# Optimization experiments

Hardware: AMD Instinct MI355X
Metric: run time of the kernel (lower is better)

## Reference

```python
import jax, jax.numpy as jnp
import numpy as np

HID, HEADS = 1024, 16
HEAD_DIM = HID // HEADS

def _rope_table(seq_len, d):
    inv_freq = 1.0 / (10000.0 ** (jnp.arange(0, d, 2, dtype=jnp.float32) / d))  # [d/2]
    sin_inp = jnp.arange(seq_len, dtype=jnp.float32)[:, None] * inv_freq[None, :]  # [S, d/2]
    return jnp.concatenate([jnp.sin(sin_inp), jnp.cos(sin_inp)], axis=-1)  # [S, d]

def _apply_rope(x, pos_emb):
    # Faithful to original: cos/sin of the (already sin/cos) pos_emb values.
    half = x.shape[-1] // 2
    x1, x2 = x[..., :half], x[..., half:]
    p1, p2 = pos_emb[..., :half], pos_emb[..., half:]
    return jnp.concatenate([x1 * jnp.cos(p1) + x2 * jnp.sin(p1),
                            x2 * jnp.cos(p2) - x1 * jnp.sin(p2)], axis=-1)

def setup_inputs() -> dict:
    key = jax.random.key(0)
    ks = jax.random.split(key, 11)
    B, S = 8, 1024
    s = 1.0 / np.sqrt(HID)
    return {
        'query': jax.random.normal(ks[0], (B, S, HID), jnp.float32),
        'key':   jax.random.normal(ks[1], (B, S, HID), jnp.float32),
        'value': jax.random.normal(ks[2], (B, S, HID), jnp.float32),
        'Wq': jax.random.normal(ks[3], (HID, HID), jnp.float32) * s,
        'bq': jax.random.normal(ks[4], (HID,), jnp.float32) * s,
        'Wk': jax.random.normal(ks[5], (HID, HID), jnp.float32) * s,
        'bk': jax.random.normal(ks[6], (HID,), jnp.float32) * s,
        'Wv': jax.random.normal(ks[7], (HID, HID), jnp.float32) * s,
        'bv': jax.random.normal(ks[8], (HID,), jnp.float32) * s,
        'Wo': jax.random.normal(ks[9], (HID, HID), jnp.float32) * s,
        'bo': jax.random.normal(ks[10], (HID,), jnp.float32) * s,
    }

def reference(query, key, value, Wq, bq, Wk, bk, Wv, bv, Wo, bo):
    B, S, _ = query.shape
    q = query @ Wq.T + bq
    k = key @ Wk.T + bk
    v = value @ Wv.T + bv
    pos_emb = _rope_table(S, HID)
    q = _apply_rope(q, pos_emb)
    k = _apply_rope(k, pos_emb)
    v = _apply_rope(v, pos_emb)  # original applies RoPE to V too
    # split heads: [B, H, S, D]
    q = q.reshape(B, S, HEADS, HEAD_DIM).transpose(0, 2, 1, 3)
    k = k.reshape(B, S, HEADS, HEAD_DIM).transpose(0, 2, 1, 3)
    v = v.reshape(B, S, HEADS, HEAD_DIM).transpose(0, 2, 1, 3)
    scale = jnp.sqrt(jnp.float32(HEAD_DIM))
    attn = jnp.einsum('bhqd,bhkd->bhqk', q, k) / scale
    attn = jax.nn.softmax(attn, axis=-1)  # dropout=0.0 (eval): identity
    x = jnp.einsum('bhqk,bhkd->bhqd', attn, v)
    x = x.transpose(0, 2, 1, 3).reshape(B, S, HID)
    return x @ Wo.T + bo
```

## Files before the change

kernel.cpp:

```cpp
#include <hip/hip_runtime.h>
#include <hip/hip_fp16.h>
#include <cmath>


typedef _Float16 f16;
typedef __attribute__((ext_vector_type(4))) _Float16 f16x4;
typedef __attribute__((ext_vector_type(8))) _Float16 f16x8;
typedef __attribute__((ext_vector_type(4))) float f32x4;

#define MFMA16(a, b, c) __builtin_amdgcn_mfma_f32_16x16x32_f16((a), (b), (c), 0, 0, 0)
#define MFMA16K16(a, b, c) __builtin_amdgcn_mfma_f32_16x16x16f16((a), (b), (c), 0, 0, 0)

__device__ __forceinline__ void g2l16(void* lds, const void* g) {
  __builtin_amdgcn_global_load_lds(
      (const __attribute__((address_space(1))) void*)g,
      (__attribute__((address_space(3))) void*)lds,
      16, 0, 0);
}

__global__ void cvt3_kernel(const float* __restrict__ a, const float* __restrict__ b,
                            const float* __restrict__ c,
                            f16* __restrict__ oa, f16* __restrict__ ob, f16* __restrict__ oc) {
  const float* src;
  f16* dst;
  if (blockIdx.y == 0) { src = a; dst = oa; }
  else if (blockIdx.y == 1) { src = b; dst = ob; }
  else { src = c; dst = oc; }
  size_t t = (size_t)blockIdx.x * 256 + threadIdx.x;
  float4 v = ((const float4*)src)[t];
  f16x4 w = { (f16)v.x, (f16)v.y, (f16)v.z, (f16)v.w };
  ((f16x4*)dst)[t] = w;
}

__global__ void cvt4_kernel(const float* __restrict__ a, const float* __restrict__ b,
                            const float* __restrict__ c, const float* __restrict__ d,
                            f16* __restrict__ oa, f16* __restrict__ ob,
                            f16* __restrict__ oc, f16* __restrict__ od) {
  const float* src;
  f16* dst;
  if (blockIdx.y == 0) { src = a; dst = oa; }
  else if (blockIdx.y == 1) { src = b; dst = ob; }
  else if (blockIdx.y == 2) { src = c; dst = oc; }
  else { src = d; dst = od; }
  size_t t = (size_t)blockIdx.x * 256 + threadIdx.x;
  float4 v = ((const float4*)src)[t];
  f16x4 w = { (f16)v.x, (f16)v.y, (f16)v.z, (f16)v.w };
  ((f16x4*)dst)[t] = w;
}

struct GemmBatch {
  const f16* A[3];
  const f16* W[3];
  const float* bias[3];
  void* O[3];
  float scale[3];
};

template <bool OUT_F16>
__global__ __launch_bounds__(256)
void gemm_f16_kernel(GemmBatch gb) {
  __shared__ __align__(16) f16 sA[128 * 64];
  __shared__ __align__(16) f16 sB[128 * 64];
  const int z = blockIdx.z;
  const f16* __restrict__ A = gb.A[z];
  const f16* __restrict__ Bw = gb.W[z];
  const float* __restrict__ bias = gb.bias[z];
  void* __restrict__ Out = gb.O[z];
  const float sc = gb.scale[z];

  const int tid = threadIdx.x;
  const int lane = tid & 63;
  const int wv = tid >> 6;
  const int l15 = lane & 15;
  const int quad = lane >> 4;

  const int flat = blockIdx.x + (blockIdx.y << 3);
  const int xcd = flat & 7;
  const int t64 = flat >> 3;
  const int m0 = (xcd * 8 + (t64 & 7)) * 128;
  const int n0 = (t64 >> 3) * 128;

  const int wm = (wv & 1) * 64;
  const int wn = (wv >> 1) * 64;

  const int srow = lane >> 3;
  const int schunk = (lane & 7) ^ srow;
  const f16* gA = A + (size_t)(m0 + wv * 32 + srow) * 1024 + schunk * 8;
  const f16* gB = Bw + (size_t)(n0 + wv * 32 + srow) * 1024 + schunk * 8;
  f16* lA = sA + (wv * 32) * 64;
  f16* lB = sB + (wv * 32) * 64;

  f32x4 acc[4][4] = {};

  for (int k0 = 0; k0 < 1024; k0 += 64) {
    __syncthreads();
#pragma unroll
    for (int j = 0; j < 4; ++j) {
      g2l16(lA + j * 8 * 64, gA + (size_t)j * 8 * 1024 + k0);
      g2l16(lB + j * 8 * 64, gB + (size_t)j * 8 * 1024 + k0);
    }
    __syncthreads();
#pragma unroll
    for (int kc = 0; kc < 2; ++kc) {
      f16x8 af[4], bf[4];
#pragma unroll
      for (int t = 0; t < 4; ++t) {
        const int swz = ((kc * 4 + quad) ^ (l15 & 7)) * 8;
        af[t] = *(const f16x8*)(sA + (wm + t * 16 + l15) * 64 + swz);
        bf[t] = *(const f16x8*)(sB + (wn + t * 16 + l15) * 64 + swz);
      }
#pragma unroll
      for (int mi = 0; mi < 4; ++mi)
#pragma unroll
        for (int ni = 0; ni < 4; ++ni)
          acc[mi][ni] = MFMA16(af[mi], bf[ni], acc[mi][ni]);
    }
  }

#pragma unroll
  for (int ni = 0; ni < 4; ++ni) {
    const int col = n0 + wn + ni * 16 + l15;
    const float bv = bias[col];
#pragma unroll
    for (int mi = 0; mi < 4; ++mi) {
      const int row0 = m0 + wm + mi * 16 + quad * 4;
#pragma unroll
      for (int r = 0; r < 4; ++r) {
        float v = (acc[mi][ni][r] + bv) * sc;
        if (OUT_F16)
          ((f16*)Out)[(size_t)(row0 + r) * 1024 + col] = (f16)v;
        else
          ((float*)Out)[(size_t)(row0 + r) * 1024 + col] = v;
      }
    }
  }
}

__global__ __launch_bounds__(256)
void rope_kernel(f16* __restrict__ q, f16* __restrict__ k,
                 const f16* __restrict__ v, f16* __restrict__ vt) {
  __shared__ f16 sT[128 * 72];
  const int t = threadIdx.x;
  const int c0 = blockIdx.x * 64;
  const int s0 = blockIdx.y * 64;
  const int b = blockIdx.z;
  const int sr = t >> 2;
  const int cq = (t & 3) * 16;
  const int s = s0 + sr;

  float c1[16], s1[16], c2[16], s2[16];
#pragma unroll
  for (int j = 0; j < 16; ++j) {
    const int i = c0 + cq + j;
    const float invf = exp2f((float)i * -0.025952563241307517f);
    const float th = (float)s * invf;
    const float p1 = sinf(th), p2 = cosf(th);
    c1[j] = __cosf(p1); s1[j] = __sinf(p1);
    c2[j] = __cosf(p2); s2[j] = __sinf(p2);
  }

  const size_t base = ((size_t)(b * 1024 + s)) * 1024 + c0 + cq;

#pragma unroll
  for (int tz = 0; tz < 2; ++tz) {
    f16* ptr = tz ? k : q;
    f16x8 x1a = *(f16x8*)(ptr + base);
    f16x8 x1b = *(f16x8*)(ptr + base + 8);
    f16x8 x2a = *(f16x8*)(ptr + base + 512);
    f16x8 x2b = *(f16x8*)(ptr + base + 520);
    f16x8 r1a, r1b, r2a, r2b;
#pragma unroll
    for (int j = 0; j < 8; ++j) {
      float a0 = (float)x1a[j], b0 = (float)x2a[j];
      float a1 = (float)x1b[j], b1 = (float)x2b[j];
      r1a[j] = (f16)(a0 * c1[j] + b0 * s1[j]);
      r2a[j] = (f16)(b0 * c2[j] - a0 * s2[j]);
      r1b[j] = (f16)(a1 * c1[8 + j] + b1 * s1[8 + j]);
      r2b[j] = (f16)(b1 * c2[8 + j] - a1 * s2[8 + j]);
    }
    *(f16x8*)(ptr + base) = r1a;
    *(f16x8*)(ptr + base + 8) = r1b;
    *(f16x8*)(ptr + base + 512) = r2a;
    *(f16x8*)(ptr + base + 520) = r2b;
  }

  {
    f16x8 x1a = *(const f16x8*)(v + base);
    f16x8 x1b = *(const f16x8*)(v + base + 8);
    f16x8 x2a = *(const f16x8*)(v + base + 512);
    f16x8 x2b = *(const f16x8*)(v + base + 520);
#pragma unroll
    for (int j = 0; j < 8; ++j) {
      float a0 = (float)x1a[j], b0 = (float)x2a[j];
      float a1 = (float)x1b[j], b1 = (float)x2b[j];
      sT[(cq + j) * 72 + sr] = (f16)(a0 * c1[j] + b0 * s1[j]);
      sT[(64 + cq + j) * 72 + sr] = (f16)(b0 * c2[j] - a0 * s2[j]);
      sT[(cq + 8 + j) * 72 + sr] = (f16)(a1 * c1[8 + j] + b1 * s1[8 + j]);
      sT[(64 + cq + 8 + j) * 72 + sr] = (f16)(b1 * c2[8 + j] - a1 * s2[8 + j]);
    }
  }
  __syncthreads();

  const int lr = t >> 1;
  const int sh = (t & 1) * 32;
  const int h = (lr < 64) ? (c0 >> 6) : (8 + (c0 >> 6));
  const int d = lr & 63;
  const size_t gbase = ((size_t)((b * 16 + h) * 64 + d)) * 1024 + s0 + sh;
#pragma unroll
  for (int m = 0; m < 4; ++m)
    *(f16x8*)(vt + gbase + m * 8) = *(const f16x8*)(sT + lr * 72 + sh + m * 8);
}

__global__ __launch_bounds__(512, 8)
void attn_kernel(const f16* __restrict__ q, const f16* __restrict__ k,
                 const f16* __restrict__ vt, f16* __restrict__ xo) {
  __shared__ __align__(16) f16 smem[16384];
  f16* sK = smem;
  f16* sV = smem + 128 * 64;
  const int tid = threadIdx.x;
  const int lane = tid & 63;
  const int wv = tid >> 6;
  const int l15 = lane & 15;
  const int quad = lane >> 4;
  const int bh = blockIdx.x;
  const int qt = blockIdx.y;
  const int b = bh >> 4, h = bh & 15;
  const size_t hidbase = ((size_t)b << 20) + (size_t)(h << 6);
  const int sq0 = qt * 128 + wv * 16;

  f16x8 fq[2];
#pragma unroll
  for (int kc = 0; kc < 2; ++kc)
    fq[kc] = *(const f16x8*)(q + hidbase + (size_t)(sq0 + l15) * 1024 + kc * 32 + quad * 8);

  f32x4 ot[4] = {};
  f32x4 ls = {};
  const f16x4 fone = { (f16)1.0f, (f16)1.0f, (f16)1.0f, (f16)1.0f };

  const int srowK = lane >> 3;
  const int schunkK = (lane & 7) ^ srowK;
  const f16* gK = k + hidbase + (size_t)(wv * 16 + srowK) * 1024 + schunkK * 8;
  const int vrow = lane >> 4;
  const f16* gVbase = vt + ((size_t)bh * 64) * 1024;

  for (int kt = 0; kt < 8; ++kt) {
    const int sk0 = kt * 128;
    __syncthreads();
#pragma unroll
    for (int j = 0; j < 2; ++j)
      g2l16(sK + (wv * 16 + j * 8) * 64, gK + (size_t)(sk0 + j * 8) * 1024);
#pragma unroll
    for (int i = 0; i < 2; ++i) {
      const int row = wv * 8 + i * 4 + vrow;
      const int gch = (lane & 15) ^ (row & 15);
      g2l16(sV + (wv * 8 + i * 4) * 128, gVbase + (size_t)row * 1024 + sk0 + gch * 8);
    }
    __syncthreads();

#pragma unroll
    for (int nj = 0; nj < 8; ++nj) {
      f32x4 st = { -12.0f, -12.0f, -12.0f, -12.0f };
#pragma unroll
      for (int kc = 0; kc < 2; ++kc) {
        f16x8 fk = *(const f16x8*)(sK + (nj * 16 + l15) * 64 +
                                   ((kc * 4 + quad) ^ (l15 & 7)) * 8);
        st = MFMA16(fk, fq[kc], st);
      }
      const float p0 = exp2f(st[0]);
      const float p1 = exp2f(st[1]);
      const float p2 = exp2f(st[2]);
      const float p3 = exp2f(st[3]);
      auto plo = __builtin_amdgcn_cvt_pkrtz(p0, p1);
      auto phi = __builtin_amdgcn_cvt_pkrtz(p2, p3);
      f16x4 pf;
      pf[0] = (f16)plo[0]; pf[1] = (f16)plo[1];
      pf[2] = (f16)phi[0]; pf[3] = (f16)phi[1];
      ls = MFMA16K16(fone, pf, ls);
#pragma unroll
      for (int nd = 0; nd < 4; ++nd) {
        f16x4 fv = *(const f16x4*)(sV + (nd * 16 + l15) * 128 +
                                   ((nj * 2 + (quad >> 1)) ^ l15) * 8 + (quad & 1) * 4);
        ot[nd] = MFMA16K16(fv, pf, ot[nd]);
      }
    }
  }

  const float inv = 1.0f / ls[0];

  __syncthreads();
  f16* sO = smem + wv * (16 * 72);
#pragma unroll
  for (int nd = 0; nd < 4; ++nd) {
    f16x4 w;
#pragma unroll
    for (int r = 0; r < 4; ++r) w[r] = (f16)(ot[nd][r] * inv);
    *(f16x4*)(sO + l15 * 72 + nd * 16 + quad * 4) = w;
  }
  const int orow = lane >> 2;
  const int oseg = (lane & 3) * 16;
  const size_t gb = hidbase + (size_t)(sq0 + orow) * 1024 + oseg;
  *(f16x8*)(xo + gb) = *(const f16x8*)(sO + orow * 72 + oseg);
  *(f16x8*)(xo + gb + 8) = *(const f16x8*)(sO + orow * 72 + oseg + 8);
}

extern "C" void kernel_launch(void* const* d_in, const int* in_sizes, int n_in,
                              void* d_out, int out_size, void* d_ws, size_t ws_size,
                              hipStream_t stream) {
  const float* query = (const float*)d_in[0];
  const float* key   = (const float*)d_in[1];
  const float* value = (const float*)d_in[2];
  const float* Wq = (const float*)d_in[3];
  const float* bq = (const float*)d_in[4];
  const float* Wk = (const float*)d_in[5];
  const float* bk = (const float*)d_in[6];
  const float* Wv = (const float*)d_in[7];
  const float* bv = (const float*)d_in[8];
  const float* Wo = (const float*)d_in[9];
  const float* bo = (const float*)d_in[10];

  char* ws = (char*)d_ws;
  const size_t SZT = (size_t)8 * 1024 * 1024 * 2;
  const size_t SZW = (size_t)1024 * 1024 * 2;
  f16* Xq  = (f16*)(ws);
  f16* Xk  = (f16*)(ws + SZT);
  f16* Xv  = (f16*)(ws + 2 * SZT);
  f16* Wqh = (f16*)(ws + 3 * SZT);
  f16* Wkh = (f16*)(ws + 3 * SZT + SZW);
  f16* Wvh = (f16*)(ws + 3 * SZT + 2 * SZW);
  f16* Woh = (f16*)(ws + 3 * SZT + 3 * SZW);
  f16* Qp  = (f16*)(ws + 3 * SZT + 4 * SZW);
  f16* Kp  = (f16*)(ws + 4 * SZT + 4 * SZW);
  f16* Vp  = (f16*)(ws + 5 * SZT + 4 * SZW);
  f16* Vt  = (f16*)(ws + 6 * SZT + 4 * SZW);
  f16* Xat = (f16*)(ws + 7 * SZT + 4 * SZW);

  cvt3_kernel<<<dim3(8192, 3), 256, 0, stream>>>(query, key, value, Xq, Xk, Xv);
  cvt4_kernel<<<dim3(1024, 4), 256, 0, stream>>>(Wq, Wk, Wv, Wo, Wqh, Wkh, Wvh, Woh);

  const float SCQ = 0.18033688011112042f;
  GemmBatch gqkv;
  gqkv.A[0] = Xq;  gqkv.A[1] = Xk;  gqkv.A[2] = Xv;
  gqkv.W[0] = Wqh; gqkv.W[1] = Wkh; gqkv.W[2] = Wvh;
  gqkv.bias[0] = bq; gqkv.bias[1] = bk; gqkv.bias[2] = bv;
  gqkv.O[0] = Qp;  gqkv.O[1] = Kp;  gqkv.O[2] = Vp;
  gqkv.scale[0] = SCQ; gqkv.scale[1] = 1.0f; gqkv.scale[2] = 1.0f;
  gemm_f16_kernel<true><<<dim3(8, 64, 3), 256, 0, stream>>>(gqkv);

  rope_kernel<<<dim3(8, 16, 8), 256, 0, stream>>>(Qp, Kp, Vp, Vt);

  attn_kernel<<<dim3(128, 8), 512, 0, stream>>>(Qp, Kp, Vt, Xat);

  GemmBatch go;
  go.A[0] = Xat; go.A[1] = nullptr; go.A[2] = nullptr;
  go.W[0] = Woh; go.W[1] = nullptr; go.W[2] = nullptr;
  go.bias[0] = bo; go.bias[1] = nullptr; go.bias[2] = nullptr;
  go.O[0] = d_out; go.O[1] = nullptr; go.O[2] = nullptr;
  go.scale[0] = 1.0f; go.scale[1] = 1.0f; go.scale[2] = 1.0f;
  gemm_f16_kernel<false><<<dim3(8, 64, 1), 256, 0, stream>>>(go);
}
```

Baseline: 329.8 us.

## Triple-buffer GEMM LDS loads and enlarge block tile to 256x128

Rewrites the projection GEMM to use 512-thread blocks computing 256x128 tiles, with a three-stage LDS ring buffer. Global-to-LDS loads are issued two k-steps ahead and waited on with explicit vmcnt counts, so memory latency overlaps with MFMA work. Fewer blocks are launched and LDS use rises to 144KB per block, which limits occupancy to one block per CU. The manual waitcnt accounting is fragile if the number of loads per stage changes.

```diff
diff --git a/kernel.cpp b/kernel.cpp
--- a/kernel.cpp
+++ b/kernel.cpp
@@ -57,10 +57,10 @@
 };
 
 template <bool OUT_F16>
-__global__ __launch_bounds__(256)
+__global__ __launch_bounds__(512, 1)
 void gemm_f16_kernel(GemmBatch gb) {
-  __shared__ __align__(16) f16 sA[128 * 64];
-  __shared__ __align__(16) f16 sB[128 * 64];
+  __shared__ __align__(16) f16 sA[3][256 * 64];
+  __shared__ __align__(16) f16 sB[3][128 * 64];
   const int z = blockIdx.z;
   const f16* __restrict__ A = gb.A[z];
   const f16* __restrict__ Bw = gb.W[z];
@@ -76,38 +76,38 @@
 
   const int flat = blockIdx.x + (blockIdx.y << 3);
   const int xcd = flat & 7;
-  const int t64 = flat >> 3;
-  const int m0 = (xcd * 8 + (t64 & 7)) * 128;
-  const int n0 = (t64 >> 3) * 128;
-
-  const int wm = (wv & 1) * 64;
-  const int wn = (wv >> 1) * 64;
+  const int t32 = flat >> 3;
+  const int m0 = (xcd * 4 + (t32 & 3)) * 256;
+  const int n0 = (t32 >> 2) * 128;
+
+  const int wm = (wv & 3) * 64;
+  const int wn = (wv >> 2) * 64;
 
   const int srow = lane >> 3;
   const int schunk = (lane & 7) ^ srow;
   const f16* gA = A + (size_t)(m0 + wv * 32 + srow) * 1024 + schunk * 8;
-  const f16* gB = Bw + (size_t)(n0 + wv * 32 + srow) * 1024 + schunk * 8;
-  f16* lA = sA + (wv * 32) * 64;
-  f16* lB = sB + (wv * 32) * 64;
+  const f16* gB = Bw + (size_t)(n0 + wv * 16 + srow) * 1024 + schunk * 8;
 
   f32x4 acc[4][4] = {};
 
-  for (int k0 = 0; k0 < 1024; k0 += 64) {
-    __syncthreads();
-#pragma unroll
-    for (int j = 0; j < 4; ++j) {
-      g2l16(lA + j * 8 * 64, gA + (size_t)j * 8 * 1024 + k0);
-      g2l16(lB + j * 8 * 64, gB + (size_t)j * 8 * 1024 + k0);
-    }
-    __syncthreads();
+  auto STAGE = [&](int t, int bi) {
+#pragma unroll
+    for (int j = 0; j < 4; ++j)
+      g2l16(&sA[bi][(wv * 32 + j * 8) * 64], gA + (size_t)j * 8 * 1024 + t * 64);
+#pragma unroll
+    for (int j = 0; j < 2; ++j)
+      g2l16(&sB[bi][(wv * 16 + j * 8) * 64], gB + (size_t)j * 8 * 1024 + t * 64);
+  };
+
+  auto COMPUTE = [&](int bi) {
 #pragma unroll
     for (int kc = 0; kc < 2; ++kc) {
       f16x8 af[4], bf[4];
 #pragma unroll
-      for (int t = 0; t < 4; ++t) {
+      for (int t4 = 0; t4 < 4; ++t4) {
         const int swz = ((kc * 4 + quad) ^ (l15 & 7)) * 8;
-        af[t] = *(const f16x8*)(sA + (wm + t * 16 + l15) * 64 + swz);
-        bf[t] = *(const f16x8*)(sB + (wn + t * 16 + l15) * 64 + swz);
+        af[t4] = *(const f16x8*)(&sA[bi][(wm + t4 * 16 + l15) * 64 + swz]);
+        bf[t4] = *(const f16x8*)(&sB[bi][(wn + t4 * 16 + l15) * 64 + swz]);
       }
 #pragma unroll
       for (int mi = 0; mi < 4; ++mi)
@@ -115,6 +115,29 @@
         for (int ni = 0; ni < 4; ++ni)
           acc[mi][ni] = MFMA16(af[mi], bf[ni], acc[mi][ni]);
     }
+  };
+
+  STAGE(0, 0);
+  STAGE(1, 1);
+  int bc = 0;
+  for (int t = 0; t < 16; ++t) {
+    __builtin_amdgcn_sched_barrier(0);
+    __builtin_amdgcn_s_barrier();
+    __builtin_amdgcn_sched_barrier(0);
+    if (t < 14) {
+      int bs = bc + 2; if (bs >= 3) bs -= 3;
+      STAGE(t + 2, bs);
+      asm volatile("s_waitcnt vmcnt(12)" ::: "memory");
+    } else if (t == 14) {
+      asm volatile("s_waitcnt vmcnt(6)" ::: "memory");
+    } else {
+      asm volatile("s_waitcnt vmcnt(0)" ::: "memory");
+    }
+    __builtin_amdgcn_sched_barrier(0);
+    __builtin_amdgcn_s_barrier();
+    __builtin_amdgcn_sched_barrier(0);
+    COMPUTE(bc);
+    ++bc; if (bc >= 3) bc -= 3;
   }
 
 #pragma unroll
@@ -344,7 +367,7 @@
   gqkv.bias[0] = bq; gqkv.bias[1] = bk; gqkv.bias[2] = bv;
   gqkv.O[0] = Qp;  gqkv.O[1] = Kp;  gqkv.O[2] = Vp;
   gqkv.scale[0] = SCQ; gqkv.scale[1] = 1.0f; gqkv.scale[2] = 1.0f;
-  gemm_f16_kernel<true><<<dim3(8, 64, 3), 256, 0, stream>>>(gqkv);
+  gemm_f16_kernel<true><<<dim3(8, 32, 3), 512, 0, stream>>>(gqkv);
 
   rope_kernel<<<dim3(8, 16, 8), 256, 0, stream>>>(Qp, Kp, Vp, Vt);
 
@@ -356,5 +379,5 @@
   go.bias[0] = bo; go.bias[1] = nullptr; go.bias[2] = nullptr;
   go.O[0] = d_out; go.O[1] = nullptr; go.O[2] = nullptr;
   go.scale[0] = 1.0f; go.scale[1] = 1.0f; go.scale[2] = 1.0f;
-  gemm_f16_kernel<false><<<dim3(8, 64, 1), 256, 0, stream>>>(go);
-}
+  gemm_f16_kernel<false><<<dim3(8, 32, 1), 512, 0, stream>>>(go);
+}
```

Result: slower. 342.0 us (+3.7%).
